# Kernel optimization log

Measured on AMD Instinct MI355X. Metric: run time of the kernel, lower is better.

Reference implementation:

```python
import jax, jax.numpy as jnp
import numpy as np

T_STEPS = 16384
N = 2048
SPIKE_THRESHOLD = 30.0
W_MEAN = 0.3
W_VAR = 0.2
E_L_VAL = -50.0
TAU_M_VAL = 1.8
TAU_G_VAL = 2.75
R_I_VAL = 67.5


def setup_inputs() -> dict:
    key = jax.random.key(0)
    k_x, k_w = jax.random.split(key)
    x_in = jax.random.normal(k_x, (T_STEPS, N), dtype=jnp.float32)
    # weights uniform in [w_mean - w_var, w_mean + w_var]
    rand_ws = W_MEAN - W_VAR + 2.0 * W_VAR * jax.random.uniform(k_w, (N, N), dtype=jnp.float32)
    n_exc = int(0.8 * N)
    signs = jnp.concatenate([jnp.ones((n_exc,)), -jnp.ones((N - n_exc,))]).astype(jnp.float32)
    w = signs[:, None] * jnp.abs(rand_ws)
    E_L = jnp.full((N,), E_L_VAL, dtype=jnp.float32)
    tau_m = jnp.full((N,), TAU_M_VAL, dtype=jnp.float32)
    R_I = jnp.full((N,), R_I_VAL, dtype=jnp.float32)
    tau_g = jnp.full((N,), TAU_G_VAL, dtype=jnp.float32)
    v0 = jnp.zeros((N,), dtype=jnp.float32)
    g0 = jnp.zeros((N,), dtype=jnp.float32)
    return {"x_in": x_in, "w": w, "E_L": E_L, "tau_m": tau_m, "R_I": R_I, "tau_g": tau_g, "v0": v0, "g0": g0}


def reference(x_in, w, E_L, tau_m, R_I, tau_g, v0, g0):
    # self-recurrence mask zeros the diagonal
    w_eff = w * (1.0 - jnp.eye(N, dtype=w.dtype))

    def step(carry, x_t):
        v, g = carry
        I = g @ w_eff + 0.9 * x_t                       # [N]
        v_next = v + (E_L - v + I * R_I) / tau_m        # Euler update
        soft_spike = jax.nn.sigmoid(v_next - SPIKE_THRESHOLD)
        spiked = (v_next >= SPIKE_THRESHOLD).astype(v.dtype)
        not_spiked = 1.0 - spiked                       # == (spiked - 1)/-1
        v_new = spiked * E_L + not_spiked * v_next      # reset to E_L on spike
        g_new = spiked + not_spiked * (g - g / tau_g)   # conductance decay / reset to 1
        return (v_new, g_new), soft_spike

    (_, _), spikes = jax.lax.scan(step, (v0, g0), x_in)
    return spikes  # [T, N] soft spike trace (module's return value per step)
```

## Files before the change

### kernel.cpp

```cpp
#include <hip/hip_runtime.h>

#define T_STEPS 16384
#define N 2048
#define COLS_PER_BLK 8
#define NBLK (N / COLS_PER_BLK)
#define THREADS 256
#define FLAG_STRIDE 16
#define FLAGS_BYTES (NBLK * FLAG_STRIDE * 4)


__global__ void __launch_bounds__(THREADS, 1)
lif_kernel(const float* __restrict__ x_in, const float* __restrict__ w,
           const float* __restrict__ E_L, const float* __restrict__ tau_m,
           const float* __restrict__ R_I, const float* __restrict__ tau_g,
           const float* __restrict__ v0,  const float* __restrict__ g0,
           float* __restrict__ out, float* gbufA, float* gbufB,
           unsigned* flags)
{
    __shared__ float w_lds[COLS_PER_BLK][N];
    __shared__ float g_lds[N];

    const int tid = threadIdx.x;
    const int blk = blockIdx.x;
    const int j0  = blk * COLS_PER_BLK;

    for (int r8 = 0; r8 < 8; ++r8) {
        int i = r8 * THREADS + tid;
        const float4* wrow = reinterpret_cast<const float4*>(w + (size_t)i * N + j0);
        float4 a = wrow[0];
        float4 b = wrow[1];
        float vals[8] = {a.x, a.y, a.z, a.w, b.x, b.y, b.z, b.w};
        #pragma unroll
        for (int jc = 0; jc < 8; ++jc)
            w_lds[jc][i] = (i == j0 + jc) ? 0.0f : vals[jc];
    }
    __syncthreads();

    const int col = tid >> 5;
    const int s   = tid & 31;
    const int j   = j0 + col;

    float4 wreg[16];
    #pragma unroll
    for (int k = 0; k < 16; ++k)
        wreg[k] = *reinterpret_cast<const float4*>(&w_lds[col][s * 4 + k * 128]);

    float v_st = 0.f, g_st = 0.f, eL = 0.f, tm = 1.f, ri = 0.f, tg = 1.f;
    if (s == 0) {
        v_st = v0[j]; g_st = g0[j];
        eL = E_L[j]; tm = tau_m[j]; ri = R_I[j]; tg = tau_g[j];
        __hip_atomic_store(&gbufA[j], g_st, __ATOMIC_RELAXED,
                           __HIP_MEMORY_SCOPE_AGENT);
    }
    __syncthreads();
    if (tid == 0)
        __hip_atomic_store(&flags[blk * FLAG_STRIDE], 1u, __ATOMIC_RELAXED,
                           __HIP_MEMORY_SCOPE_AGENT);

    float xv = (s == 0) ? x_in[j] : 0.f;

    for (int t = 0; t < T_STEPS; ++t) {
        const float* gsrc = (t & 1) ? gbufB : gbufA;
        float*       gdst = (t & 1) ? gbufA : gbufB;

        if (tid < 64) {
            const unsigned tgt = (unsigned)(t + 1);
            for (;;) {
                unsigned f0 = __hip_atomic_load(&flags[(tid      ) * FLAG_STRIDE],
                                                __ATOMIC_RELAXED, __HIP_MEMORY_SCOPE_AGENT);
                unsigned f1 = __hip_atomic_load(&flags[(tid +  64) * FLAG_STRIDE],
                                                __ATOMIC_RELAXED, __HIP_MEMORY_SCOPE_AGENT);
                unsigned f2 = __hip_atomic_load(&flags[(tid + 128) * FLAG_STRIDE],
                                                __ATOMIC_RELAXED, __HIP_MEMORY_SCOPE_AGENT);
                unsigned f3 = __hip_atomic_load(&flags[(tid + 192) * FLAG_STRIDE],
                                                __ATOMIC_RELAXED, __HIP_MEMORY_SCOPE_AGENT);
                unsigned fm = min(min(f0, f1), min(f2, f3));
                if (__all(fm >= tgt)) break;
                __builtin_amdgcn_s_sleep(1);
            }
        }
        __syncthreads();

        float gv[8];
        #pragma unroll
        for (int u = 0; u < 8; ++u)
            gv[u] = __hip_atomic_load((const float*)&gsrc[tid + u * 256],
                                      __ATOMIC_RELAXED, __HIP_MEMORY_SCOPE_AGENT);
        #pragma unroll
        for (int u = 0; u < 8; ++u)
            g_lds[tid + u * 256] = gv[u];
        __syncthreads();

        float4 acc = {0.f, 0.f, 0.f, 0.f};
        #pragma unroll
        for (int k = 0; k < 16; ++k) {
            float4 g4 = *reinterpret_cast<const float4*>(&g_lds[s * 4 + k * 128]);
            acc.x = fmaf(wreg[k].x, g4.x, acc.x);
            acc.y = fmaf(wreg[k].y, g4.y, acc.y);
            acc.z = fmaf(wreg[k].z, g4.z, acc.z);
            acc.w = fmaf(wreg[k].w, g4.w, acc.w);
        }
        float sum = (acc.x + acc.y) + (acc.z + acc.w);
        #pragma unroll
        for (int m = 16; m >= 1; m >>= 1)
            sum += __shfl_xor(sum, m, 64);

        float soft = 0.f;
        if (s == 0) {
            float I      = fmaf(0.9f, xv, sum);
            float v_next = v_st + (eL - v_st + I * ri) / tm;
            soft         = 1.0f / (1.0f + expf(30.0f - v_next));
            bool  spiked = v_next >= 30.0f;
            v_st = spiked ? eL : v_next;
            g_st = spiked ? 1.0f : (g_st - g_st / tg);
            __hip_atomic_store(&gdst[j], g_st, __ATOMIC_RELAXED,
                               __HIP_MEMORY_SCOPE_AGENT);
        }
        __syncthreads();

        if (tid == 0)
            __hip_atomic_store(&flags[blk * FLAG_STRIDE], (unsigned)(t + 2),
                               __ATOMIC_RELAXED, __HIP_MEMORY_SCOPE_AGENT);

        if (s == 0) {
            out[(size_t)t * N + j] = soft;
            if (t + 1 < T_STEPS) xv = x_in[(size_t)(t + 1) * N + j];
        }
    }
}

extern "C" void kernel_launch(void* const* d_in, const int* in_sizes, int n_in,
                              void* d_out, int out_size, void* d_ws, size_t ws_size,
                              hipStream_t stream) {
    const float* x_in  = (const float*)d_in[0];
    const float* w     = (const float*)d_in[1];
    const float* E_L   = (const float*)d_in[2];
    const float* tau_m = (const float*)d_in[3];
    const float* R_I   = (const float*)d_in[4];
    const float* tau_g = (const float*)d_in[5];
    const float* v0    = (const float*)d_in[6];
    const float* g0    = (const float*)d_in[7];
    float* out = (float*)d_out;

    unsigned* flags = (unsigned*)d_ws;
    float* gA = (float*)((char*)d_ws + FLAGS_BYTES);
    float* gB = (float*)((char*)d_ws + FLAGS_BYTES + N * sizeof(float));

    hipMemsetAsync(d_ws, 0, FLAGS_BYTES, stream);

    void* args[] = {(void*)&x_in, (void*)&w, (void*)&E_L, (void*)&tau_m,
                    (void*)&R_I, (void*)&tau_g, (void*)&v0, (void*)&g0,
                    (void*)&out, (void*)&gA, (void*)&gB, (void*)&flags};
    hipLaunchCooperativeKernel((const void*)lif_kernel, dim3(NBLK), dim3(THREADS),
                               args, 0, stream);
}
```

Baseline: 41.12 ms.

## Replace per-block flag barrier with step-tagged g slots polled directly

Each g value is now written as a 64-bit word that carries the step number in its upper half. The words sit in a 4-deep ring of slots, and each wave polls the g values it needs directly until every tag matches. This removes the separate flag publish/poll phase and two of the per-step __syncthreads. The LDS g buffer is double-buffered, and the work layout changes to one wave computing two columns with a full 64-lane reduction. The cost is more polling traffic, since every thread spins on global memory without sleeping, and the slot ring grows to 64 KB.

```diff
diff --git a/kernel.cpp b/kernel.cpp
--- a/kernel.cpp
+++ b/kernel.cpp
@@ -2,11 +2,11 @@
 
 #define T_STEPS 16384
 #define N 2048
-#define COLS_PER_BLK 8
-#define NBLK (N / COLS_PER_BLK)
+#define NBLK 256
 #define THREADS 256
-#define FLAG_STRIDE 16
-#define FLAGS_BYTES (NBLK * FLAG_STRIDE * 4)
+#define NSLOT 4
+
+typedef unsigned long long u64;
 
 
 __global__ void __launch_bounds__(THREADS, 1)
@@ -14,21 +14,19 @@
            const float* __restrict__ E_L, const float* __restrict__ tau_m,
            const float* __restrict__ R_I, const float* __restrict__ tau_g,
            const float* __restrict__ v0,  const float* __restrict__ g0,
-           float* __restrict__ out, float* gbufA, float* gbufB,
-           unsigned* flags)
+           float* __restrict__ out, u64* __restrict__ slots)
 {
-    __shared__ float w_lds[COLS_PER_BLK][N];
-    __shared__ float g_lds[N];
+    __shared__ float w_lds[8][N];
+    __shared__ float g_lds[2][N];
 
     const int tid = threadIdx.x;
     const int blk = blockIdx.x;
-    const int j0  = blk * COLS_PER_BLK;
+    const int j0  = blk * 8;
 
     for (int r8 = 0; r8 < 8; ++r8) {
         int i = r8 * THREADS + tid;
         const float4* wrow = reinterpret_cast<const float4*>(w + (size_t)i * N + j0);
-        float4 a = wrow[0];
-        float4 b = wrow[1];
+        float4 a = wrow[0], b = wrow[1];
         float vals[8] = {a.x, a.y, a.z, a.w, b.x, b.y, b.z, b.w};
         #pragma unroll
         for (int jc = 0; jc < 8; ++jc)
@@ -36,95 +34,89 @@
     }
     __syncthreads();
 
-    const int col = tid >> 5;
-    const int s   = tid & 31;
-    const int j   = j0 + col;
+    const int wv = tid >> 6;
+    const int ln = tid & 63;
+    const int cA = 2 * wv;
+    const int cB = 2 * wv + 1;
 
     float4 wreg[16];
     #pragma unroll
-    for (int k = 0; k < 16; ++k)
-        wreg[k] = *reinterpret_cast<const float4*>(&w_lds[col][s * 4 + k * 128]);
+    for (int u = 0; u < 16; ++u) {
+        int r = 2 * ln + 128 * u;
+        wreg[u].x = w_lds[cA][r];  wreg[u].y = w_lds[cA][r + 1];
+        wreg[u].z = w_lds[cB][r];  wreg[u].w = w_lds[cB][r + 1];
+    }
 
-    float v_st = 0.f, g_st = 0.f, eL = 0.f, tm = 1.f, ri = 0.f, tg = 1.f;
-    if (s == 0) {
-        v_st = v0[j]; g_st = g0[j];
-        eL = E_L[j]; tm = tau_m[j]; ri = R_I[j]; tg = tau_g[j];
-        __hip_atomic_store(&gbufA[j], g_st, __ATOMIC_RELAXED,
-                           __HIP_MEMORY_SCOPE_AGENT);
+    const bool own  = (ln == 0) || (ln == 32);
+    const int  jown = j0 + ((ln == 0) ? cA : cB);
+
+    float v_st = 0.f, g_st = 0.f, eL = 0.f, tm = 1.f, ri = 0.f, tg = 1.f, xv = 0.f;
+    if (own) {
+        v_st = v0[jown]; g_st = g0[jown];
+        eL = E_L[jown]; tm = tau_m[jown]; ri = R_I[jown]; tg = tau_g[jown];
+        xv = x_in[jown];
+        __hip_atomic_store(&slots[jown],
+                           ((u64)1u << 32) | (u64)__float_as_uint(g_st),
+                           __ATOMIC_RELAXED, __HIP_MEMORY_SCOPE_AGENT);
     }
-    __syncthreads();
-    if (tid == 0)
-        __hip_atomic_store(&flags[blk * FLAG_STRIDE], 1u, __ATOMIC_RELAXED,
-                           __HIP_MEMORY_SCOPE_AGENT);
-
-    float xv = (s == 0) ? x_in[j] : 0.f;
 
     for (int t = 0; t < T_STEPS; ++t) {
-        const float* gsrc = (t & 1) ? gbufB : gbufA;
-        float*       gdst = (t & 1) ? gbufA : gbufB;
+        const u64* slot = slots + (size_t)(t & 3) * N;
+        const unsigned tgt = (unsigned)(t + 1);
+        float gp[8];
+        for (;;) {
+            bool ok = true;
+            #pragma unroll
+            for (int u = 0; u < 4; ++u) {
+                int j = 512 * wv + 2 * ln + 128 * u;
+                u64 p0 = __hip_atomic_load(&slot[j],     __ATOMIC_RELAXED,
+                                           __HIP_MEMORY_SCOPE_AGENT);
+                u64 p1 = __hip_atomic_load(&slot[j + 1], __ATOMIC_RELAXED,
+                                           __HIP_MEMORY_SCOPE_AGENT);
+                ok = ok && ((unsigned)(p0 >> 32) == tgt)
+                        && ((unsigned)(p1 >> 32) == tgt);
+                gp[2 * u]     = __uint_as_float((unsigned)p0);
+                gp[2 * u + 1] = __uint_as_float((unsigned)p1);
+            }
+            if (__all(ok)) break;
+        }
 
-        if (tid < 64) {
-            const unsigned tgt = (unsigned)(t + 1);
-            for (;;) {
-                unsigned f0 = __hip_atomic_load(&flags[(tid      ) * FLAG_STRIDE],
-                                                __ATOMIC_RELAXED, __HIP_MEMORY_SCOPE_AGENT);
-                unsigned f1 = __hip_atomic_load(&flags[(tid +  64) * FLAG_STRIDE],
-                                                __ATOMIC_RELAXED, __HIP_MEMORY_SCOPE_AGENT);
-                unsigned f2 = __hip_atomic_load(&flags[(tid + 128) * FLAG_STRIDE],
-                                                __ATOMIC_RELAXED, __HIP_MEMORY_SCOPE_AGENT);
-                unsigned f3 = __hip_atomic_load(&flags[(tid + 192) * FLAG_STRIDE],
-                                                __ATOMIC_RELAXED, __HIP_MEMORY_SCOPE_AGENT);
-                unsigned fm = min(min(f0, f1), min(f2, f3));
-                if (__all(fm >= tgt)) break;
-                __builtin_amdgcn_s_sleep(1);
-            }
+        float* gl = g_lds[t & 1];
+        #pragma unroll
+        for (int u = 0; u < 4; ++u) {
+            int j = 512 * wv + 2 * ln + 128 * u;
+            *reinterpret_cast<float2*>(&gl[j]) = make_float2(gp[2*u], gp[2*u+1]);
         }
         __syncthreads();
 
-        float gv[8];
+        float accA = 0.f, accB = 0.f;
         #pragma unroll
-        for (int u = 0; u < 8; ++u)
-            gv[u] = __hip_atomic_load((const float*)&gsrc[tid + u * 256],
-                                      __ATOMIC_RELAXED, __HIP_MEMORY_SCOPE_AGENT);
+        for (int u = 0; u < 16; ++u) {
+            int r = 2 * ln + 128 * u;
+            float2 g2 = *reinterpret_cast<const float2*>(&gl[r]);
+            accA = fmaf(wreg[u].x, g2.x, fmaf(wreg[u].y, g2.y, accA));
+            accB = fmaf(wreg[u].z, g2.x, fmaf(wreg[u].w, g2.y, accB));
+        }
         #pragma unroll
-        for (int u = 0; u < 8; ++u)
-            g_lds[tid + u * 256] = gv[u];
-        __syncthreads();
+        for (int m = 1; m <= 32; m <<= 1) {
+            accA += __shfl_xor(accA, m, 64);
+            accB += __shfl_xor(accB, m, 64);
+        }
 
-        float4 acc = {0.f, 0.f, 0.f, 0.f};
-        #pragma unroll
-        for (int k = 0; k < 16; ++k) {
-            float4 g4 = *reinterpret_cast<const float4*>(&g_lds[s * 4 + k * 128]);
-            acc.x = fmaf(wreg[k].x, g4.x, acc.x);
-            acc.y = fmaf(wreg[k].y, g4.y, acc.y);
-            acc.z = fmaf(wreg[k].z, g4.z, acc.z);
-            acc.w = fmaf(wreg[k].w, g4.w, acc.w);
-        }
-        float sum = (acc.x + acc.y) + (acc.z + acc.w);
-        #pragma unroll
-        for (int m = 16; m >= 1; m >>= 1)
-            sum += __shfl_xor(sum, m, 64);
-
-        float soft = 0.f;
-        if (s == 0) {
+        if (own) {
+            float sum    = (ln == 0) ? accA : accB;
             float I      = fmaf(0.9f, xv, sum);
             float v_next = v_st + (eL - v_st + I * ri) / tm;
-            soft         = 1.0f / (1.0f + expf(30.0f - v_next));
+            float soft   = 1.0f / (1.0f + expf(30.0f - v_next));
             bool  spiked = v_next >= 30.0f;
             v_st = spiked ? eL : v_next;
             g_st = spiked ? 1.0f : (g_st - g_st / tg);
-            __hip_atomic_store(&gdst[j], g_st, __ATOMIC_RELAXED,
-                               __HIP_MEMORY_SCOPE_AGENT);
-        }
-        __syncthreads();
-
-        if (tid == 0)
-            __hip_atomic_store(&flags[blk * FLAG_STRIDE], (unsigned)(t + 2),
+            __hip_atomic_store(&slots[(size_t)((t + 1) & 3) * N + jown],
+                               ((u64)(unsigned)(t + 2) << 32) |
+                               (u64)__float_as_uint(g_st),
                                __ATOMIC_RELAXED, __HIP_MEMORY_SCOPE_AGENT);
-
-        if (s == 0) {
-            out[(size_t)t * N + j] = soft;
-            if (t + 1 < T_STEPS) xv = x_in[(size_t)(t + 1) * N + j];
+            out[(size_t)t * N + jown] = soft;
+            if (t + 1 < T_STEPS) xv = x_in[(size_t)(t + 1) * N + jown];
         }
     }
 }
@@ -142,15 +134,13 @@
     const float* g0    = (const float*)d_in[7];
     float* out = (float*)d_out;
 
-    unsigned* flags = (unsigned*)d_ws;
-    float* gA = (float*)((char*)d_ws + FLAGS_BYTES);
-    float* gB = (float*)((char*)d_ws + FLAGS_BYTES + N * sizeof(float));
+    u64* slots = (u64*)d_ws;
 
-    hipMemsetAsync(d_ws, 0, FLAGS_BYTES, stream);
+    hipMemsetAsync(d_ws, 0, NSLOT * N * sizeof(u64), stream);
 
     void* args[] = {(void*)&x_in, (void*)&w, (void*)&E_L, (void*)&tau_m,
                     (void*)&R_I, (void*)&tau_g, (void*)&v0, (void*)&g0,
-                    (void*)&out, (void*)&gA, (void*)&gB, (void*)&flags};
+                    (void*)&out, (void*)&slots};
     hipLaunchCooperativeKernel((const void*)lif_kernel, dim3(NBLK), dim3(THREADS),
                                args, 0, stream);
 }
```

Measured after the change: 61.43 ms. 49.4% more time.

## Replace flag barrier with sign-bit epoch-tagged data slots for inter-block sync

Applied to the files above, without the earlier changes.

Removes the separate per-block flag array and its polling barrier. Each conductance value is written into one of four rotating slots with an epoch bit in its sign, so readers spin directly on the data they need using nontemporal, cache-bypassing loads. Two of the three per-step __syncthreads go away, g_lds is double-buffered, and weights are read from LDS each step instead of living in registers. The scheme relies on g always being non-negative so the sign bit is free, and it adds LDS traffic for the weights.

```diff
diff --git a/kernel.cpp b/kernel.cpp
--- a/kernel.cpp
+++ b/kernel.cpp
@@ -2,11 +2,11 @@
 
 #define T_STEPS 16384
 #define N 2048
-#define COLS_PER_BLK 8
-#define NBLK (N / COLS_PER_BLK)
+#define NBLK 256
 #define THREADS 256
-#define FLAG_STRIDE 16
-#define FLAGS_BYTES (NBLK * FLAG_STRIDE * 4)
+#define NSLOT 4
+
+typedef float f32x4 __attribute__((ext_vector_type(4)));
 
 
 __global__ void __launch_bounds__(THREADS, 1)
@@ -14,22 +14,20 @@
            const float* __restrict__ E_L, const float* __restrict__ tau_m,
            const float* __restrict__ R_I, const float* __restrict__ tau_g,
            const float* __restrict__ v0,  const float* __restrict__ g0,
-           float* __restrict__ out, float* gbufA, float* gbufB,
-           unsigned* flags)
+           float* __restrict__ out, unsigned* __restrict__ slots)
 {
-    __shared__ float w_lds[COLS_PER_BLK][N];
-    __shared__ float g_lds[N];
+    __shared__ float w_lds[8][N];
+    __shared__ float g_lds[2][N];
 
     const int tid = threadIdx.x;
     const int blk = blockIdx.x;
-    const int j0  = blk * COLS_PER_BLK;
+    const int j0  = blk * 8;
 
     for (int r8 = 0; r8 < 8; ++r8) {
         int i = r8 * THREADS + tid;
         const float4* wrow = reinterpret_cast<const float4*>(w + (size_t)i * N + j0);
-        float4 a = wrow[0];
-        float4 b = wrow[1];
-        float vals[8] = {a.x, a.y, a.z, a.w, b.x, b.y, b.z, b.w};
+        float4 a4 = wrow[0], b4 = wrow[1];
+        float vals[8] = {a4.x, a4.y, a4.z, a4.w, b4.x, b4.y, b4.z, b4.w};
         #pragma unroll
         for (int jc = 0; jc < 8; ++jc)
             w_lds[jc][i] = (i == j0 + jc) ? 0.0f : vals[jc];
@@ -40,89 +38,74 @@
     const int s   = tid & 31;
     const int j   = j0 + col;
 
-    float4 wreg[16];
-    #pragma unroll
-    for (int k = 0; k < 16; ++k)
-        wreg[k] = *reinterpret_cast<const float4*>(&w_lds[col][s * 4 + k * 128]);
-
-    float v_st = 0.f, g_st = 0.f, eL = 0.f, tm = 1.f, ri = 0.f, tg = 1.f;
+    float v_st = 0.f, g_st = 0.f, eL = 0.f, tm = 1.f, ri = 0.f, tg = 1.f, xv = 0.f;
     if (s == 0) {
         v_st = v0[j]; g_st = g0[j];
         eL = E_L[j]; tm = tau_m[j]; ri = R_I[j]; tg = tau_g[j];
-        __hip_atomic_store(&gbufA[j], g_st, __ATOMIC_RELAXED,
-                           __HIP_MEMORY_SCOPE_AGENT);
+        xv = x_in[j];
+        __hip_atomic_store(&slots[j], __float_as_uint(g_st),
+                           __ATOMIC_RELAXED, __HIP_MEMORY_SCOPE_AGENT);
     }
-    __syncthreads();
-    if (tid == 0)
-        __hip_atomic_store(&flags[blk * FLAG_STRIDE], 1u, __ATOMIC_RELAXED,
-                           __HIP_MEMORY_SCOPE_AGENT);
-
-    float xv = (s == 0) ? x_in[j] : 0.f;
 
     for (int t = 0; t < T_STEPS; ++t) {
-        const float* gsrc = (t & 1) ? gbufB : gbufA;
-        float*       gdst = (t & 1) ? gbufA : gbufB;
+        const unsigned* slot = slots + (size_t)(t & 3) * N;
+        const unsigned  es   = (((unsigned)t >> 2) & 1u) << 31;
 
-        if (tid < 64) {
-            const unsigned tgt = (unsigned)(t + 1);
-            for (;;) {
-                unsigned f0 = __hip_atomic_load(&flags[(tid      ) * FLAG_STRIDE],
-                                                __ATOMIC_RELAXED, __HIP_MEMORY_SCOPE_AGENT);
-                unsigned f1 = __hip_atomic_load(&flags[(tid +  64) * FLAG_STRIDE],
-                                                __ATOMIC_RELAXED, __HIP_MEMORY_SCOPE_AGENT);
-                unsigned f2 = __hip_atomic_load(&flags[(tid + 128) * FLAG_STRIDE],
-                                                __ATOMIC_RELAXED, __HIP_MEMORY_SCOPE_AGENT);
-                unsigned f3 = __hip_atomic_load(&flags[(tid + 192) * FLAG_STRIDE],
-                                                __ATOMIC_RELAXED, __HIP_MEMORY_SCOPE_AGENT);
-                unsigned fm = min(min(f0, f1), min(f2, f3));
-                if (__all(fm >= tgt)) break;
-                __builtin_amdgcn_s_sleep(1);
-            }
+        const unsigned* p = slot + tid * 8;
+        f32x4 a, b;
+        for (;;) {
+            asm volatile(
+                "global_load_dwordx4 %0, %2, off sc0 sc1 nt\n\t"
+                "global_load_dwordx4 %1, %2, off offset:16 sc0 sc1 nt\n\t"
+                "s_waitcnt vmcnt(0)"
+                : "=&v"(a), "=&v"(b)
+                : "v"(p)
+                : "memory");
+            unsigned mm = (__float_as_uint(a[0]) ^ es) | (__float_as_uint(a[1]) ^ es)
+                        | (__float_as_uint(a[2]) ^ es) | (__float_as_uint(a[3]) ^ es)
+                        | (__float_as_uint(b[0]) ^ es) | (__float_as_uint(b[1]) ^ es)
+                        | (__float_as_uint(b[2]) ^ es) | (__float_as_uint(b[3]) ^ es);
+            if (!(mm & 0x80000000u)) break;
         }
-        __syncthreads();
 
-        float gv[8];
+        float* gl = g_lds[t & 1];
+        f32x4 ca, cb;
         #pragma unroll
-        for (int u = 0; u < 8; ++u)
-            gv[u] = __hip_atomic_load((const float*)&gsrc[tid + u * 256],
-                                      __ATOMIC_RELAXED, __HIP_MEMORY_SCOPE_AGENT);
-        #pragma unroll
-        for (int u = 0; u < 8; ++u)
-            g_lds[tid + u * 256] = gv[u];
+        for (int c = 0; c < 4; ++c) {
+            ca[c] = __uint_as_float(__float_as_uint(a[c]) & 0x7FFFFFFFu);
+            cb[c] = __uint_as_float(__float_as_uint(b[c]) & 0x7FFFFFFFu);
+        }
+        *reinterpret_cast<f32x4*>(&gl[tid * 8])     = ca;
+        *reinterpret_cast<f32x4*>(&gl[tid * 8 + 4]) = cb;
         __syncthreads();
 
         float4 acc = {0.f, 0.f, 0.f, 0.f};
         #pragma unroll
         for (int k = 0; k < 16; ++k) {
-            float4 g4 = *reinterpret_cast<const float4*>(&g_lds[s * 4 + k * 128]);
-            acc.x = fmaf(wreg[k].x, g4.x, acc.x);
-            acc.y = fmaf(wreg[k].y, g4.y, acc.y);
-            acc.z = fmaf(wreg[k].z, g4.z, acc.z);
-            acc.w = fmaf(wreg[k].w, g4.w, acc.w);
+            int r = s * 4 + k * 128;
+            float4 g4 = *reinterpret_cast<const float4*>(&gl[r]);
+            float4 w4 = *reinterpret_cast<const float4*>(&w_lds[col][r]);
+            acc.x = fmaf(w4.x, g4.x, acc.x);
+            acc.y = fmaf(w4.y, g4.y, acc.y);
+            acc.z = fmaf(w4.z, g4.z, acc.z);
+            acc.w = fmaf(w4.w, g4.w, acc.w);
         }
         float sum = (acc.x + acc.y) + (acc.z + acc.w);
         #pragma unroll
         for (int m = 16; m >= 1; m >>= 1)
             sum += __shfl_xor(sum, m, 64);
 
-        float soft = 0.f;
         if (s == 0) {
             float I      = fmaf(0.9f, xv, sum);
             float v_next = v_st + (eL - v_st + I * ri) / tm;
-            soft         = 1.0f / (1.0f + expf(30.0f - v_next));
+            float soft   = 1.0f / (1.0f + expf(30.0f - v_next));
             bool  spiked = v_next >= 30.0f;
             v_st = spiked ? eL : v_next;
             g_st = spiked ? 1.0f : (g_st - g_st / tg);
-            __hip_atomic_store(&gdst[j], g_st, __ATOMIC_RELAXED,
-                               __HIP_MEMORY_SCOPE_AGENT);
-        }
-        __syncthreads();
-
-        if (tid == 0)
-            __hip_atomic_store(&flags[blk * FLAG_STRIDE], (unsigned)(t + 2),
+            unsigned Sn  = (((unsigned)(t + 1) >> 2) & 1u) << 31;
+            __hip_atomic_store(&slots[(size_t)((t + 1) & 3) * N + j],
+                               __float_as_uint(g_st) | Sn,
                                __ATOMIC_RELAXED, __HIP_MEMORY_SCOPE_AGENT);
-
-        if (s == 0) {
             out[(size_t)t * N + j] = soft;
             if (t + 1 < T_STEPS) xv = x_in[(size_t)(t + 1) * N + j];
         }
@@ -142,15 +125,13 @@
     const float* g0    = (const float*)d_in[7];
     float* out = (float*)d_out;
 
-    unsigned* flags = (unsigned*)d_ws;
-    float* gA = (float*)((char*)d_ws + FLAGS_BYTES);
-    float* gB = (float*)((char*)d_ws + FLAGS_BYTES + N * sizeof(float));
+    unsigned* slots = (unsigned*)d_ws;
 
-    hipMemsetAsync(d_ws, 0, FLAGS_BYTES, stream);
+    hipMemsetAsync(d_ws, 0xAA, NSLOT * N * sizeof(unsigned), stream);
 
     void* args[] = {(void*)&x_in, (void*)&w, (void*)&E_L, (void*)&tau_m,
                     (void*)&R_I, (void*)&tau_g, (void*)&v0, (void*)&g0,
-                    (void*)&out, (void*)&gA, (void*)&gB, (void*)&flags};
+                    (void*)&out, (void*)&slots};
     hipLaunchCooperativeKernel((const void*)lif_kernel, dim3(NBLK), dim3(THREADS),
                                args, 0, stream);
 }
```

New measurement: 121.5 ms. 196% more time.
